# Kernel tuning notes

Measured on AMD Instinct MI355X. Metric: run time of the kernel, lower is better.

The kernel has to match this reference:

```python
import jax, jax.numpy as jnp
import numpy as np

TEMPERATURE = 0.07
EPS = 1e-08
HARD_NEG_WEIGHT = 2.0
DOMAIN_SEP_WEIGHT = 1.5


def setup_inputs() -> dict:
    key = jax.random.key(0)
    k1, k2, k3 = jax.random.split(key, 3)
    B, L, D = 32, 256, 256
    feats = jax.random.normal(k1, (B, L, D), dtype=jnp.float32)
    dataset_ids = jax.random.randint(k2, (B, L), 0, 4, dtype=jnp.int64 if jax.config.read('jax_enable_x64') else jnp.int32)
    image_ids = jax.random.randint(k3, (B, L), 0, 128, dtype=jnp.int64 if jax.config.read('jax_enable_x64') else jnp.int32)
    return {"feats": feats, "dataset_ids": dataset_ids, "image_ids": image_ids}


def reference(feats, dataset_ids, image_ids):
    B, L, D = feats.shape
    N = B * L
    x = feats.reshape(N, D)
    # F.normalize: x / clamp_min(||x||, eps)
    x = x / jnp.maximum(jnp.linalg.norm(x, axis=-1, keepdims=True), EPS)
    sim = jnp.matmul(x, x.T) / TEMPERATURE  # [N, N]

    did = dataset_ids.reshape(-1)
    iid = image_ids.reshape(-1)
    same_img = (did[:, None] == did[None, :]) & (iid[:, None] == iid[None, :])
    eye = jnp.eye(N, dtype=bool)
    pos_mask = same_img & ~eye
    diff_dataset = did[:, None] != did[None, :]

    sim_exp = jnp.exp(sim)

    # global 0.8-quantile over cross-dataset similarities (linear interpolation, as torch.quantile)
    q = jnp.nanquantile(jnp.where(diff_dataset, sim, jnp.nan), 0.8)
    thr = jnp.where(diff_dataset.any(), q, 0.0)
    hard_neg_mask = diff_dataset & (sim > thr)

    neg_weights = jnp.where(diff_dataset, DOMAIN_SEP_WEIGHT, 1.0) * jnp.where(hard_neg_mask, HARD_NEG_WEIGHT, 1.0)

    pos_sum = jnp.sum(sim_exp * pos_mask.astype(sim.dtype), axis=1)
    # note: ~pos_mask includes the diagonal, matching the torch code
    neg_sum = jnp.sum(sim_exp * neg_weights * (~pos_mask).astype(sim.dtype), axis=1)

    loss = -jnp.log((pos_sum + EPS) / (pos_sum + neg_sum + EPS))

    valid = pos_mask.any(axis=1)
    n_valid = valid.sum()
    masked_mean = jnp.sum(loss * valid.astype(loss.dtype)) / jnp.maximum(n_valid, 1).astype(loss.dtype)
    return jnp.where(n_valid > 0, masked_mean, loss.mean())
```

## Files before the change

kernel.cpp:

```cpp
#include <hip/hip_runtime.h>
#include <math.h>

#define N_TOK 8192
#define DIM   256
#define INV_T 14.285714285714286f
#define RANGE 14.2857142857f
#define EPS   1e-8f
#define NBINS 8192
#define LOG2E 1.44269504f

typedef __attribute__((ext_vector_type(4))) float f32x4;

#define OFF_P     0
#define P_BYTES   (N_TOK * DIM)
#define OFF_PP    (OFF_P + P_BYTES)
#define OFF_PN    (OFF_PP + 64 * N_TOK * 4)
#define OFF_HIST  (OFF_PN + 64 * N_TOK * 4)
#define OFF_THR   (OFF_HIST + NBINS * 4)

#define GLOBAL_AS __attribute__((address_space(1)))
#define LDS_AS    __attribute__((address_space(3)))

#define ROWB 272
#define SLOTS_PER_MAT (128 * 17)
#define STAGE_CALLS (2 * SLOTS_PER_MAT / 64)

__device__ __forceinline__ void tri_decode(int b, int& it, int& jt) {
    int i_low = (int)((sqrtf(8.f * (float)b + 1.f) - 1.f) * 0.5f);
    while ((i_low + 1) * (i_low + 2) / 2 <= b) ++i_low;
    while (i_low * (i_low + 1) / 2 > b) --i_low;
    const int j_low = b - i_low * (i_low + 1) / 2;
    it = 63 - i_low; jt = 63 - j_low;
}

__global__ __launch_bounds__(256) void k_prep(const float* __restrict__ feats,
                                              unsigned int* __restrict__ Pq) {
    const int row = blockIdx.x * 4 + (threadIdx.x >> 6);
    const int l = threadIdx.x & 63;
    const float4 v = *reinterpret_cast<const float4*>(&feats[(size_t)row * DIM + l * 4]);
    float s = v.x * v.x + v.y * v.y + v.z * v.z + v.w * v.w;
#pragma unroll
    for (int m = 1; m <= 32; m <<= 1) s += __shfl_xor(s, m);
    const float r = 1.0f / fmaxf(sqrtf(s), EPS);
    int pk = __builtin_amdgcn_cvt_pk_fp8_f32(v.x * r, v.y * r, 0, false);
    pk = __builtin_amdgcn_cvt_pk_fp8_f32(v.z * r, v.w * r, pk, true);
    Pq[row * 64 + l] = (unsigned int)pk;
}

__device__ __forceinline__ void stage_and_gemm(
    const char* __restrict__ Pq, int iBase, int jBase,
    char* At, char* Bt, int tid, f32x4 (&acc)[2][4]) {
    const int w = tid >> 6, l = tid & 63;
    for (int k = w; k < STAGE_CALLS; k += 8) {
        const int s0 = k * 64;
        const int isB = (s0 >= SLOTS_PER_MAT);
        const int r0 = s0 - (isB ? SLOTS_PER_MAT : 0);
        const int sl = r0 + l;
        const int row = sl / 17;
        const int col = sl - row * 17;
        const int gb = isB ? jBase : iBase;
        const char* src = Pq + (size_t)(gb + row) * DIM + (col & 15) * 16;
        char* dst = (isB ? Bt : At) + (size_t)r0 * 16;
        __builtin_amdgcn_global_load_lds((const GLOBAL_AS unsigned int*)src,
                                         (LDS_AS unsigned int*)dst, 16, 0, 0);
    }
    __syncthreads();

    const int wr = w >> 1, wc = w & 1;
    const int g = l >> 4, p = l & 15;
    const char* a0 = At + (wr * 32 + p) * ROWB + g * 8;
    const char* b0 = Bt + (wc * 64 + p) * ROWB + g * 8;
#pragma unroll
    for (int c = 0; c < 8; ++c) {
        const int off = c * 32;
        const long af0 = *(const long*)(a0 + off);
        const long af1 = *(const long*)(a0 + 16 * ROWB + off);
        const long bf0 = *(const long*)(b0 + off);
        const long bf1 = *(const long*)(b0 + 16 * ROWB + off);
        const long bf2 = *(const long*)(b0 + 32 * ROWB + off);
        const long bf3 = *(const long*)(b0 + 48 * ROWB + off);
        acc[0][0] = __builtin_amdgcn_mfma_f32_16x16x32_fp8_fp8(af0, bf0, acc[0][0], 0, 0, 0);
        acc[0][1] = __builtin_amdgcn_mfma_f32_16x16x32_fp8_fp8(af0, bf1, acc[0][1], 0, 0, 0);
        acc[0][2] = __builtin_amdgcn_mfma_f32_16x16x32_fp8_fp8(af0, bf2, acc[0][2], 0, 0, 0);
        acc[0][3] = __builtin_amdgcn_mfma_f32_16x16x32_fp8_fp8(af0, bf3, acc[0][3], 0, 0, 0);
        acc[1][0] = __builtin_amdgcn_mfma_f32_16x16x32_fp8_fp8(af1, bf0, acc[1][0], 0, 0, 0);
        acc[1][1] = __builtin_amdgcn_mfma_f32_16x16x32_fp8_fp8(af1, bf1, acc[1][1], 0, 0, 0);
        acc[1][2] = __builtin_amdgcn_mfma_f32_16x16x32_fp8_fp8(af1, bf2, acc[1][2], 0, 0, 0);
        acc[1][3] = __builtin_amdgcn_mfma_f32_16x16x32_fp8_fp8(af1, bf3, acc[1][3], 0, 0, 0);
    }
}

__global__ __launch_bounds__(512, 2) void k_hist(
    const char* __restrict__ Pq, const int* __restrict__ did,
    unsigned int* __restrict__ hist) {
    int it, jt;
    tri_decode(blockIdx.x * 32, it, jt);
    const int iBase = it * 128, jBase = jt * 128;
    const bool diag = (it == jt);

    __shared__ char At[SLOTS_PER_MAT * 16];
    __shared__ char Bt[SLOTS_PER_MAT * 16];
    __shared__ int dA[128], dB[128];
    __shared__ unsigned int h[NBINS];

    const int tid = threadIdx.x;
    if (tid < 128) dA[tid] = did[iBase + tid];
    else if (tid < 256) dB[tid - 128] = did[jBase + tid - 128];
    for (int i = tid; i < NBINS; i += 512) h[i] = 0;

    f32x4 acc[2][4];
#pragma unroll
    for (int a = 0; a < 2; a++)
#pragma unroll
        for (int c = 0; c < 4; c++) acc[a][c] = (f32x4){0.f, 0.f, 0.f, 0.f};

    stage_and_gemm(Pq, iBase, jBase, At, Bt, tid, acc);

    const int w = tid >> 6, l = tid & 63;
    const int wr = w >> 1, wc = w & 1;
    const int g = l >> 4, p = l & 15;
    int dRow[2][4];
#pragma unroll
    for (int fm = 0; fm < 2; ++fm)
#pragma unroll
        for (int q = 0; q < 4; ++q) dRow[fm][q] = dA[wr * 32 + fm * 16 + g * 4 + q];

    const unsigned int wgt = diag ? 1u : 2u;
    const float binScale = (float)NBINS / (2.0f * RANGE);
    const float K1 = INV_T * binScale, K0 = RANGE * binScale;
#pragma unroll
    for (int fn = 0; fn < 4; ++fn) {
        const int dcol = dB[wc * 64 + fn * 16 + p];
#pragma unroll
        for (int fm = 0; fm < 2; ++fm)
#pragma unroll
            for (int q = 0; q < 4; ++q) {
                if (dRow[fm][q] != dcol) {
                    int bn = (int)fmaf(acc[fm][fn][q], K1, K0);
                    bn = min(max(bn, 0), NBINS - 1);
                    atomicAdd(&h[bn], wgt);
                }
            }
    }
    __syncthreads();
    for (int i = tid; i < NBINS; i += 512) {
        unsigned int c = h[i];
        if (c) atomicAdd(&hist[i], c);
    }
}

__global__ __launch_bounds__(512, 4) void k_main(
    const char* __restrict__ Pq,
    const int* __restrict__ did, const int* __restrict__ iid,
    const float* __restrict__ thrp,
    float* __restrict__ partP, float* __restrict__ partN) {
    int it, jt;
    tri_decode(blockIdx.x, it, jt);
    const int iBase = it * 128, jBase = jt * 128;
    const bool diag = (it == jt);

    __shared__ char At[SLOTS_PER_MAT * 16];
    __shared__ char Bt[SLOTS_PER_MAT * 16];
    __shared__ int dA[128], kA[128], dB[128], kB[128];
    __shared__ float rbT[2][128], rbP[2][128];
    __shared__ float cbT[4][128], cbP[4][128];

    const int tid = threadIdx.x;
    if (tid < 128) {
        int d = did[iBase + tid], i2 = iid[iBase + tid];
        dA[tid] = d; kA[tid] = (d << 16) | i2;
    } else if (tid < 256) {
        int r = tid - 128;
        int d = did[jBase + r], i2 = iid[jBase + r];
        dB[r] = d; kB[r] = (d << 16) | i2;
    }

    f32x4 acc[2][4];
#pragma unroll
    for (int a = 0; a < 2; a++)
#pragma unroll
        for (int c = 0; c < 4; c++) acc[a][c] = (f32x4){0.f, 0.f, 0.f, 0.f};

    stage_and_gemm(Pq, iBase, jBase, At, Bt, tid, acc);

    const int w = tid >> 6, l = tid & 63;
    const int wr = w >> 1, wc = w & 1;
    const int g = l >> 4, p = l & 15;

    int dRow[2][4], kRow[2][4], selfRow[2][4];
#pragma unroll
    for (int fm = 0; fm < 2; ++fm)
#pragma unroll
        for (int q = 0; q < 4; ++q) {
            const int rIdx = wr * 32 + fm * 16 + g * 4 + q;
            dRow[fm][q] = dA[rIdx];
            kRow[fm][q] = kA[rIdx];
            selfRow[fm][q] = diag ? rIdx : -1;
        }

    const float CE = INV_T * LOG2E;
    const float thr2 = thrp[0] * LOG2E;
    const float E_DIAG = __builtin_amdgcn_exp2f(CE);
    float tR[2][4], pR[2][4], tC[4], pC[4];
#pragma unroll
    for (int a = 0; a < 4; a++) { tC[a] = 0.f; pC[a] = 0.f; }
#pragma unroll
    for (int a = 0; a < 2; a++)
#pragma unroll
        for (int c = 0; c < 4; c++) { tR[a][c] = 0.f; pR[a][c] = 0.f; }

#pragma unroll
    for (int fn = 0; fn < 4; ++fn) {
        const int cIdx = wc * 64 + fn * 16 + p;
        const int dcol = dB[cIdx], kcol = kB[cIdx];
#pragma unroll
        for (int fm = 0; fm < 2; ++fm)
#pragma unroll
            for (int q = 0; q < 4; ++q) {
                const float tt = acc[fm][fn][q] * CE;
                float e = __builtin_amdgcn_exp2f(tt);
                const bool self = (selfRow[fm][q] == cIdx);
                e = self ? E_DIAG : e;
                const float w1 = (tt > thr2) ? 3.0f : 1.5f;
                const float wg = (dRow[fm][q] != dcol) ? w1 : 1.0f;
                tR[fm][q] = fmaf(e, wg, tR[fm][q]);
                tC[fn] = fmaf(e, wg, tC[fn]);
                const bool pos = (kRow[fm][q] == kcol) && !self;
                const float ep = pos ? e : 0.f;
                pR[fm][q] += ep;
                pC[fn] += ep;
            }
    }
#pragma unroll
    for (int m = 1; m <= 8; m <<= 1)
#pragma unroll
        for (int a = 0; a < 2; a++)
#pragma unroll
            for (int c = 0; c < 4; c++) {
                tR[a][c] += __shfl_xor(tR[a][c], m);
                pR[a][c] += __shfl_xor(pR[a][c], m);
            }
#pragma unroll
    for (int m = 16; m <= 32; m <<= 1)
#pragma unroll
        for (int a = 0; a < 4; a++) {
            tC[a] += __shfl_xor(tC[a], m);
            pC[a] += __shfl_xor(pC[a], m);
        }
    float tv = 0.f, pv = 0.f;
#pragma unroll
    for (int fm = 0; fm < 2; ++fm)
#pragma unroll
        for (int q = 0; q < 4; ++q)
            if (p == fm * 4 + q) { tv = tR[fm][q]; pv = pR[fm][q]; }

    if (p < 8) {
        const int rowLocal = (p >> 2) * 16 + g * 4 + (p & 3);
        rbT[wc][wr * 32 + rowLocal] = tv;
        rbP[wc][wr * 32 + rowLocal] = pv;
    }
    if (l < 16) {
#pragma unroll
        for (int fn = 0; fn < 4; ++fn) {
            cbT[wr][wc * 64 + fn * 16 + l] = tC[fn];
            cbP[wr][wc * 64 + fn * 16 + l] = pC[fn];
        }
    }
    __syncthreads();
    if (tid < 128) {
        const float T = rbT[0][tid] + rbT[1][tid];
        const float Pp = rbP[0][tid] + rbP[1][tid];
        const size_t off = (size_t)jt * N_TOK + iBase + tid;
        partP[off] = Pp;
        partN[off] = T - Pp;
    } else if (tid < 256 && !diag) {
        const int c = tid - 128;
        const float T = cbT[0][c] + cbT[1][c] + cbT[2][c] + cbT[3][c];
        const float Pp = cbP[0][c] + cbP[1][c] + cbP[2][c] + cbP[3][c];
        const size_t off = (size_t)it * N_TOK + jBase + c;
        partP[off] = Pp;
        partN[off] = T - Pp;
    }
}

__global__ __launch_bounds__(1024) void k_thr(const unsigned int* __restrict__ hist,
                                              float* __restrict__ thrp) {
    __shared__ unsigned long long scan[1024];
    const int t = threadIdx.x;
    const int CHUNK = NBINS / 1024;
    const int base = t * CHUNK;
    unsigned long long own = 0;
    for (int i = 0; i < CHUNK; i++) own += hist[base + i];
    scan[t] = own;
    __syncthreads();
    for (int o = 1; o < 1024; o <<= 1) {
        unsigned long long v = (t >= o) ? scan[t - o] : 0ULL;
        __syncthreads();
        scan[t] += v;
        __syncthreads();
    }
    unsigned long long total = scan[1023];
    if (total == 0) {
        if (t == 0) thrp[0] = 0.f;
        return;
    }
    unsigned long long k1 = (4ULL * (total - 1)) / 5ULL;
    unsigned long long rem = (4ULL * (total - 1)) % 5ULL;
    float frac = (float)rem * 0.2f;
    unsigned long long k2 = (k1 + 1 < total) ? k1 + 1 : k1;
    __shared__ float vk[2];
    unsigned long long cumBefore = scan[t] - own;
    const float binw = 2.0f * RANGE / (float)NBINS;
    for (int which = 0; which < 2; which++) {
        unsigned long long k = which ? k2 : k1;
        if (cumBefore <= k && k < scan[t]) {
            unsigned long long c = cumBefore;
            int bin = base;
            for (int i = 0; i < CHUNK; i++) {
                c += hist[base + i];
                if (c > k) { bin = base + i; break; }
            }
            vk[which] = -RANGE + ((float)bin + 0.5f) * binw;
        }
    }
    __syncthreads();
    if (t == 0) thrp[0] = vk[0] + frac * (vk[1] - vk[0]);
}

__global__ __launch_bounds__(256) void k_reduce(const float* __restrict__ pp,
                                                const float* __restrict__ pn,
                                                float* __restrict__ acc) {
    const int t = threadIdx.x;
    const int r = blockIdx.x * 128 + (t & 127);
    const int jh = t >> 7;
    float sp = 0.f, sn = 0.f;
    const float* bp = pp + (size_t)jh * 32 * N_TOK + r;
    const float* bn = pn + (size_t)jh * 32 * N_TOK + r;
#pragma unroll 8
    for (int j = 0; j < 32; ++j) {
        sp += bp[(size_t)j * N_TOK];
        sn += bn[(size_t)j * N_TOK];
    }
    __shared__ float shp[128], shn[128];
    if (jh) { shp[t & 127] = sp; shn[t & 127] = sn; }
    __syncthreads();
    float sumV = 0.f, sumA = 0.f, cnt = 0.f;
    if (!jh) {
        const float p = sp + shp[t];
        const float n = sn + shn[t];
        const float loss = -logf((p + EPS) / (p + n + EPS));
        sumA = loss;
        if (p > 0.f) { sumV = loss; cnt = 1.f; }
    }
#pragma unroll
    for (int m = 1; m <= 32; m <<= 1) {
        sumV += __shfl_xor(sumV, m);
        sumA += __shfl_xor(sumA, m);
        cnt += __shfl_xor(cnt, m);
    }
    __shared__ float wv[4], wa[4], wn[4];
    if ((t & 63) == 0) { wv[t >> 6] = sumV; wa[t >> 6] = sumA; wn[t >> 6] = cnt; }
    __syncthreads();
    if (t == 0) {
        atomicAdd(&acc[0], wv[0] + wv[1] + wv[2] + wv[3]);
        atomicAdd(&acc[1], wa[0] + wa[1] + wa[2] + wa[3]);
        atomicAdd(&acc[2], wn[0] + wn[1] + wn[2] + wn[3]);
    }
}

__global__ __launch_bounds__(64) void k_last(const float* __restrict__ acc,
                                             float* __restrict__ out) {
    if (threadIdx.x == 0) {
        const float nv = acc[2];
        out[0] = (nv > 0.f) ? (acc[0] / fmaxf(nv, 1.f)) : (acc[1] / (float)N_TOK);
    }
}

extern "C" void kernel_launch(void* const* d_in, const int* in_sizes, int n_in,
                              void* d_out, int out_size, void* d_ws, size_t ws_size,
                              hipStream_t stream) {
    (void)in_sizes; (void)n_in; (void)out_size; (void)ws_size;
    const float* feats = (const float*)d_in[0];
    const int* did = (const int*)d_in[1];
    const int* iid = (const int*)d_in[2];
    char* ws = (char*)d_ws;
    char* Pq = ws + OFF_P;
    float* partP = (float*)(ws + OFF_PP);
    float* partN = (float*)(ws + OFF_PN);
    unsigned int* hist = (unsigned int*)(ws + OFF_HIST);
    float* thrp = (float*)(ws + OFF_THR);
    float* accum = (float*)(ws + OFF_THR + 16);

    hipMemsetAsync(ws + OFF_HIST, 0, NBINS * 4 + 256, stream);
    k_prep<<<N_TOK / 4, 256, 0, stream>>>(feats, (unsigned int*)Pq);
    k_hist<<<65, 512, 0, stream>>>(Pq, did, hist);
    k_thr<<<1, 1024, 0, stream>>>(hist, thrp);
    k_main<<<64 * 65 / 2, 512, 0, stream>>>(Pq, did, iid, thrp, partP, partN);
    k_reduce<<<64, 256, 0, stream>>>(partP, partN, accum);
    k_last<<<1, 64, 0, stream>>>(accum, (float*)d_out);
}
```

Measured before the change: 72.92 us.

## Fold temperature scale into fp8 quantization and widen LDS fragment loads

The prep kernel now scales normalized features by sqrt(CE) before fp8 conversion and permutes the k-layout so each lane can read 16-byte LDS fragments feeding two MFMAs. This removes the per-element multiply by the temperature constant in the epilogue. The main kernel gets a separate branch for off-diagonal tiles that skips self-masking logic, reuses the staging LDS for reduction buffers, and drops its occupancy hint from 4 to 2. Pre-scaling the features into larger fp8 magnitudes changes quantization error and range, and the histogram bin mapping is rescaled to match.

```diff
diff --git a/kernel.cpp b/kernel.cpp
--- a/kernel.cpp
+++ b/kernel.cpp
@@ -8,6 +8,8 @@
 #define EPS   1e-8f
 #define NBINS 8192
 #define LOG2E 1.44269504f
+#define CE    (INV_T * LOG2E)
+#define SCALE_F 4.539816f
 
 typedef __attribute__((ext_vector_type(4))) float f32x4;
 
@@ -41,10 +43,11 @@
     float s = v.x * v.x + v.y * v.y + v.z * v.z + v.w * v.w;
 #pragma unroll
     for (int m = 1; m <= 32; m <<= 1) s += __shfl_xor(s, m);
-    const float r = 1.0f / fmaxf(sqrtf(s), EPS);
+    const float r = SCALE_F / fmaxf(sqrtf(s), EPS);
     int pk = __builtin_amdgcn_cvt_pk_fp8_f32(v.x * r, v.y * r, 0, false);
     pk = __builtin_amdgcn_cvt_pk_fp8_f32(v.z * r, v.w * r, pk, true);
-    Pq[row * 64 + l] = (unsigned int)pk;
+    const int c = l >> 3, g = (l >> 1) & 3, e = l & 1;
+    Pq[row * 64 + g * 16 + c * 2 + e] = (unsigned int)pk;
 }
 
 __device__ __forceinline__ void stage_and_gemm(
@@ -68,25 +71,33 @@
 
     const int wr = w >> 1, wc = w & 1;
     const int g = l >> 4, p = l & 15;
-    const char* a0 = At + (wr * 32 + p) * ROWB + g * 8;
-    const char* b0 = Bt + (wc * 64 + p) * ROWB + g * 8;
-#pragma unroll
-    for (int c = 0; c < 8; ++c) {
-        const int off = c * 32;
-        const long af0 = *(const long*)(a0 + off);
-        const long af1 = *(const long*)(a0 + 16 * ROWB + off);
-        const long bf0 = *(const long*)(b0 + off);
-        const long bf1 = *(const long*)(b0 + 16 * ROWB + off);
-        const long bf2 = *(const long*)(b0 + 32 * ROWB + off);
-        const long bf3 = *(const long*)(b0 + 48 * ROWB + off);
-        acc[0][0] = __builtin_amdgcn_mfma_f32_16x16x32_fp8_fp8(af0, bf0, acc[0][0], 0, 0, 0);
-        acc[0][1] = __builtin_amdgcn_mfma_f32_16x16x32_fp8_fp8(af0, bf1, acc[0][1], 0, 0, 0);
-        acc[0][2] = __builtin_amdgcn_mfma_f32_16x16x32_fp8_fp8(af0, bf2, acc[0][2], 0, 0, 0);
-        acc[0][3] = __builtin_amdgcn_mfma_f32_16x16x32_fp8_fp8(af0, bf3, acc[0][3], 0, 0, 0);
-        acc[1][0] = __builtin_amdgcn_mfma_f32_16x16x32_fp8_fp8(af1, bf0, acc[1][0], 0, 0, 0);
-        acc[1][1] = __builtin_amdgcn_mfma_f32_16x16x32_fp8_fp8(af1, bf1, acc[1][1], 0, 0, 0);
-        acc[1][2] = __builtin_amdgcn_mfma_f32_16x16x32_fp8_fp8(af1, bf2, acc[1][2], 0, 0, 0);
-        acc[1][3] = __builtin_amdgcn_mfma_f32_16x16x32_fp8_fp8(af1, bf3, acc[1][3], 0, 0, 0);
+    const char* a0 = At + (wr * 32 + p) * ROWB + g * 64;
+    const char* b0 = Bt + (wc * 64 + p) * ROWB + g * 64;
+#pragma unroll
+    for (int cp = 0; cp < 4; ++cp) {
+        const int off = cp * 16;
+        const long2 aA = *(const long2*)(a0 + off);
+        const long2 aB2 = *(const long2*)(a0 + 16 * ROWB + off);
+        const long2 bA = *(const long2*)(b0 + off);
+        const long2 bB2 = *(const long2*)(b0 + 16 * ROWB + off);
+        const long2 bC = *(const long2*)(b0 + 32 * ROWB + off);
+        const long2 bD = *(const long2*)(b0 + 48 * ROWB + off);
+        acc[0][0] = __builtin_amdgcn_mfma_f32_16x16x32_fp8_fp8(aA.x, bA.x, acc[0][0], 0, 0, 0);
+        acc[0][1] = __builtin_amdgcn_mfma_f32_16x16x32_fp8_fp8(aA.x, bB2.x, acc[0][1], 0, 0, 0);
+        acc[0][2] = __builtin_amdgcn_mfma_f32_16x16x32_fp8_fp8(aA.x, bC.x, acc[0][2], 0, 0, 0);
+        acc[0][3] = __builtin_amdgcn_mfma_f32_16x16x32_fp8_fp8(aA.x, bD.x, acc[0][3], 0, 0, 0);
+        acc[1][0] = __builtin_amdgcn_mfma_f32_16x16x32_fp8_fp8(aB2.x, bA.x, acc[1][0], 0, 0, 0);
+        acc[1][1] = __builtin_amdgcn_mfma_f32_16x16x32_fp8_fp8(aB2.x, bB2.x, acc[1][1], 0, 0, 0);
+        acc[1][2] = __builtin_amdgcn_mfma_f32_16x16x32_fp8_fp8(aB2.x, bC.x, acc[1][2], 0, 0, 0);
+        acc[1][3] = __builtin_amdgcn_mfma_f32_16x16x32_fp8_fp8(aB2.x, bD.x, acc[1][3], 0, 0, 0);
+        acc[0][0] = __builtin_amdgcn_mfma_f32_16x16x32_fp8_fp8(aA.y, bA.y, acc[0][0], 0, 0, 0);
+        acc[0][1] = __builtin_amdgcn_mfma_f32_16x16x32_fp8_fp8(aA.y, bB2.y, acc[0][1], 0, 0, 0);
+        acc[0][2] = __builtin_amdgcn_mfma_f32_16x16x32_fp8_fp8(aA.y, bC.y, acc[0][2], 0, 0, 0);
+        acc[0][3] = __builtin_amdgcn_mfma_f32_16x16x32_fp8_fp8(aA.y, bD.y, acc[0][3], 0, 0, 0);
+        acc[1][0] = __builtin_amdgcn_mfma_f32_16x16x32_fp8_fp8(aB2.y, bA.y, acc[1][0], 0, 0, 0);
+        acc[1][1] = __builtin_amdgcn_mfma_f32_16x16x32_fp8_fp8(aB2.y, bB2.y, acc[1][1], 0, 0, 0);
+        acc[1][2] = __builtin_amdgcn_mfma_f32_16x16x32_fp8_fp8(aB2.y, bC.y, acc[1][2], 0, 0, 0);
+        acc[1][3] = __builtin_amdgcn_mfma_f32_16x16x32_fp8_fp8(aB2.y, bD.y, acc[1][3], 0, 0, 0);
     }
 }
 
@@ -98,8 +109,8 @@
     const int iBase = it * 128, jBase = jt * 128;
     const bool diag = (it == jt);
 
-    __shared__ char At[SLOTS_PER_MAT * 16];
-    __shared__ char Bt[SLOTS_PER_MAT * 16];
+    __shared__ __align__(16) char At[SLOTS_PER_MAT * 16];
+    __shared__ __align__(16) char Bt[SLOTS_PER_MAT * 16];
     __shared__ int dA[128], dB[128];
     __shared__ unsigned int h[NBINS];
 
@@ -126,8 +137,8 @@
         for (int q = 0; q < 4; ++q) dRow[fm][q] = dA[wr * 32 + fm * 16 + g * 4 + q];
 
     const unsigned int wgt = diag ? 1u : 2u;
-    const float binScale = (float)NBINS / (2.0f * RANGE);
-    const float K1 = INV_T * binScale, K0 = RANGE * binScale;
+    const float K1H = ((float)NBINS / (2.0f * RANGE)) / LOG2E;
+    const float K0 = 0.5f * (float)NBINS;
 #pragma unroll
     for (int fn = 0; fn < 4; ++fn) {
         const int dcol = dB[wc * 64 + fn * 16 + p];
@@ -136,7 +147,7 @@
 #pragma unroll
             for (int q = 0; q < 4; ++q) {
                 if (dRow[fm][q] != dcol) {
-                    int bn = (int)fmaf(acc[fm][fn][q], K1, K0);
+                    int bn = (int)fmaf(acc[fm][fn][q], K1H, K0);
                     bn = min(max(bn, 0), NBINS - 1);
                     atomicAdd(&h[bn], wgt);
                 }
@@ -149,7 +160,7 @@
     }
 }
 
-__global__ __launch_bounds__(512, 4) void k_main(
+__global__ __launch_bounds__(512, 2) void k_main(
     const char* __restrict__ Pq,
     const int* __restrict__ did, const int* __restrict__ iid,
     const float* __restrict__ thrp,
@@ -159,13 +170,15 @@
     const int iBase = it * 128, jBase = jt * 128;
     const bool diag = (it == jt);
 
-    __shared__ char At[SLOTS_PER_MAT * 16];
-    __shared__ char Bt[SLOTS_PER_MAT * 16];
+    __shared__ __align__(16) char At[SLOTS_PER_MAT * 16];
+    __shared__ __align__(16) char Bt[SLOTS_PER_MAT * 16];
     __shared__ int dA[128], kA[128], dB[128], kB[128];
-    __shared__ float rbT[2][128], rbP[2][128];
-    __shared__ float cbT[4][128], cbP[4][128];
 
     const int tid = threadIdx.x;
+    const int w = tid >> 6, l = tid & 63;
+    const int wr = w >> 1, wc = w & 1;
+    const int g = l >> 4, p = l & 15;
+
     if (tid < 128) {
         int d = did[iBase + tid], i2 = iid[iBase + tid];
         dA[tid] = d; kA[tid] = (d << 16) | i2;
@@ -182,12 +195,9 @@
         for (int c = 0; c < 4; c++) acc[a][c] = (f32x4){0.f, 0.f, 0.f, 0.f};
 
     stage_and_gemm(Pq, iBase, jBase, At, Bt, tid, acc);
-
-    const int w = tid >> 6, l = tid & 63;
-    const int wr = w >> 1, wc = w & 1;
-    const int g = l >> 4, p = l & 15;
-
-    int dRow[2][4], kRow[2][4], selfRow[2][4];
+    __syncthreads();
+
+    int dRow[2][4], kRow[2][4];
 #pragma unroll
     for (int fm = 0; fm < 2; ++fm)
 #pragma unroll
@@ -195,10 +205,8 @@
             const int rIdx = wr * 32 + fm * 16 + g * 4 + q;
             dRow[fm][q] = dA[rIdx];
             kRow[fm][q] = kA[rIdx];
-            selfRow[fm][q] = diag ? rIdx : -1;
-        }
-
-    const float CE = INV_T * LOG2E;
+        }
+
     const float thr2 = thrp[0] * LOG2E;
     const float E_DIAG = __builtin_amdgcn_exp2f(CE);
     float tR[2][4], pR[2][4], tC[4], pC[4];
@@ -209,27 +217,49 @@
 #pragma unroll
         for (int c = 0; c < 4; c++) { tR[a][c] = 0.f; pR[a][c] = 0.f; }
 
-#pragma unroll
-    for (int fn = 0; fn < 4; ++fn) {
-        const int cIdx = wc * 64 + fn * 16 + p;
-        const int dcol = dB[cIdx], kcol = kB[cIdx];
-#pragma unroll
-        for (int fm = 0; fm < 2; ++fm)
-#pragma unroll
-            for (int q = 0; q < 4; ++q) {
-                const float tt = acc[fm][fn][q] * CE;
-                float e = __builtin_amdgcn_exp2f(tt);
-                const bool self = (selfRow[fm][q] == cIdx);
-                e = self ? E_DIAG : e;
-                const float w1 = (tt > thr2) ? 3.0f : 1.5f;
-                const float wg = (dRow[fm][q] != dcol) ? w1 : 1.0f;
-                tR[fm][q] = fmaf(e, wg, tR[fm][q]);
-                tC[fn] = fmaf(e, wg, tC[fn]);
-                const bool pos = (kRow[fm][q] == kcol) && !self;
-                const float ep = pos ? e : 0.f;
-                pR[fm][q] += ep;
-                pC[fn] += ep;
-            }
+    if (!diag) {
+#pragma unroll
+        for (int fn = 0; fn < 4; ++fn) {
+            const int cIdx = wc * 64 + fn * 16 + p;
+            const int dcol = dB[cIdx], kcol = kB[cIdx];
+#pragma unroll
+            for (int fm = 0; fm < 2; ++fm)
+#pragma unroll
+                for (int q = 0; q < 4; ++q) {
+                    const float tt = acc[fm][fn][q];
+                    const float e = __builtin_amdgcn_exp2f(tt);
+                    const float w1 = (tt > thr2) ? 3.0f : 1.5f;
+                    const float wg = (dRow[fm][q] != dcol) ? w1 : 1.0f;
+                    tR[fm][q] = fmaf(e, wg, tR[fm][q]);
+                    tC[fn] = fmaf(e, wg, tC[fn]);
+                    const float ep = (kRow[fm][q] == kcol) ? e : 0.f;
+                    pR[fm][q] += ep;
+                    pC[fn] += ep;
+                }
+        }
+    } else {
+#pragma unroll
+        for (int fn = 0; fn < 4; ++fn) {
+            const int cIdx = wc * 64 + fn * 16 + p;
+            const int dcol = dB[cIdx], kcol = kB[cIdx];
+#pragma unroll
+            for (int fm = 0; fm < 2; ++fm)
+#pragma unroll
+                for (int q = 0; q < 4; ++q) {
+                    const int rIdx = wr * 32 + fm * 16 + g * 4 + q;
+                    const float tt = acc[fm][fn][q];
+                    float e = __builtin_amdgcn_exp2f(tt);
+                    const bool self = (rIdx == cIdx);
+                    e = self ? E_DIAG : e;
+                    const float w1 = (tt > thr2) ? 3.0f : 1.5f;
+                    const float wg = (dRow[fm][q] != dcol) ? w1 : 1.0f;
+                    tR[fm][q] = fmaf(e, wg, tR[fm][q]);
+                    tC[fn] = fmaf(e, wg, tC[fn]);
+                    const float ep = ((kRow[fm][q] == kcol) && !self) ? e : 0.f;
+                    pR[fm][q] += ep;
+                    pC[fn] += ep;
+                }
+        }
     }
 #pragma unroll
     for (int m = 1; m <= 8; m <<= 1)
@@ -254,29 +284,33 @@
         for (int q = 0; q < 4; ++q)
             if (p == fm * 4 + q) { tv = tR[fm][q]; pv = pR[fm][q]; }
 
+    float* rbT = (float*)Bt;
+    float* rbP = rbT + 256;
+    float* cbT = rbP + 256;
+    float* cbP = cbT + 512;
     if (p < 8) {
         const int rowLocal = (p >> 2) * 16 + g * 4 + (p & 3);
-        rbT[wc][wr * 32 + rowLocal] = tv;
-        rbP[wc][wr * 32 + rowLocal] = pv;
+        rbT[wc * 128 + wr * 32 + rowLocal] = tv;
+        rbP[wc * 128 + wr * 32 + rowLocal] = pv;
     }
     if (l < 16) {
 #pragma unroll
         for (int fn = 0; fn < 4; ++fn) {
-            cbT[wr][wc * 64 + fn * 16 + l] = tC[fn];
-            cbP[wr][wc * 64 + fn * 16 + l] = pC[fn];
+            cbT[wr * 128 + wc * 64 + fn * 16 + l] = tC[fn];
+            cbP[wr * 128 + wc * 64 + fn * 16 + l] = pC[fn];
         }
     }
     __syncthreads();
     if (tid < 128) {
-        const float T = rbT[0][tid] + rbT[1][tid];
-        const float Pp = rbP[0][tid] + rbP[1][tid];
+        const float T = rbT[tid] + rbT[128 + tid];
+        const float Pp = rbP[tid] + rbP[128 + tid];
         const size_t off = (size_t)jt * N_TOK + iBase + tid;
         partP[off] = Pp;
         partN[off] = T - Pp;
     } else if (tid < 256 && !diag) {
         const int c = tid - 128;
-        const float T = cbT[0][c] + cbT[1][c] + cbT[2][c] + cbT[3][c];
-        const float Pp = cbP[0][c] + cbP[1][c] + cbP[2][c] + cbP[3][c];
+        const float T = cbT[c] + cbT[128 + c] + cbT[256 + c] + cbT[384 + c];
+        const float Pp = cbP[c] + cbP[128 + c] + cbP[256 + c] + cbP[384 + c];
         const size_t off = (size_t)it * N_TOK + jBase + c;
         partP[off] = Pp;
         partN[off] = T - Pp;
```

Measured after the change: 83.06 us. 13.9% more time.
